# Kernel optimization log

Hardware: AMD Instinct MI355X
Metric: run time of the kernel (lower is better)

The kernel has to match this reference:

```python
import jax, jax.numpy as jnp
import numpy as np

B, T, C = 2, 2048, 2048
N_HEAD, N_GROUPS, HEAD_SIZE = 16, 4, 128
Q_PER_KV = N_HEAD // N_GROUPS  # 4
N_ELEM = HEAD_SIZE  # rotary_percentage = 1.0
HIDDEN = 4 * C
EPS = 1e-5


def layernorm(x, w, b):
    m = jnp.mean(x, axis=-1, keepdims=True)
    v = jnp.mean(jnp.square(x - m), axis=-1, keepdims=True)
    return (x - m) * jax.lax.rsqrt(v + EPS) * w + b


def apply_rope(x, cos, sin):
    # x: [B, H, T, n_elem]; cos/sin: [T, n_elem] (broadcast over B, H)
    d = x.shape[-1]
    x1, x2 = x[..., : d // 2], x[..., d // 2 :]
    rotated = jnp.concatenate((-x2, x1), axis=-1)
    return x * cos + rotated * sin


def setup_inputs() -> dict:
    key = jax.random.key(0)
    ks = jax.random.split(key, 8)
    x = jax.random.normal(ks[0], (B, T, C), dtype=jnp.float32)
    # rope cache (NeoX/LLaMA half-rotation layout), base 10000
    theta = 1.0 / (10000.0 ** (jnp.arange(0, N_ELEM, 2, dtype=jnp.float32) / N_ELEM))
    idx_theta = jnp.outer(jnp.arange(T, dtype=jnp.float32), theta)  # [T, n_elem//2]
    idx_theta = jnp.concatenate((idx_theta, idx_theta), axis=-1)    # [T, n_elem]
    cos, sin = jnp.cos(idx_theta), jnp.sin(idx_theta)
    mask = jnp.tril(jnp.ones((T, T), dtype=bool))[None, None]  # causal [1,1,T,T]
    s = 0.02
    return {
        "x": x,
        "cos": cos,
        "sin": sin,
        "ln1_w": jnp.ones((C,), jnp.float32),
        "ln1_b": jnp.zeros((C,), jnp.float32),
        "ln2_w": jnp.ones((C,), jnp.float32),
        "ln2_b": jnp.zeros((C,), jnp.float32),
        "w_attn": jax.random.normal(ks[1], (C, (N_HEAD + 2 * N_GROUPS) * HEAD_SIZE), jnp.float32) * s,
        "w_proj": jax.random.normal(ks[2], (C, C), jnp.float32) * s,
        "w_fc": jax.random.normal(ks[3], (C, HIDDEN), jnp.float32) * s,
        "w_mlp_proj": jax.random.normal(ks[4], (HIDDEN, C), jnp.float32) * s,
        "mask": mask,
    }


def reference(x, cos, sin, ln1_w, ln1_b, ln2_w, ln2_b, w_attn, w_proj, w_fc, w_mlp_proj, mask):
    n1 = layernorm(x, ln1_w, ln1_b)
    # fused QKV projection
    qkv = n1 @ w_attn  # [B, T, (H + 2G) * hs]
    qkv = qkv.reshape(B, T, N_GROUPS, Q_PER_KV + 2, HEAD_SIZE)
    q = qkv[:, :, :, :Q_PER_KV]      # [B, T, G, qpk, hs]
    k = qkv[:, :, :, Q_PER_KV]       # [B, T, G, hs]
    v = qkv[:, :, :, Q_PER_KV + 1]   # [B, T, G, hs]
    # q -> [B, H, T, hs] (group-major head order)
    q = q.transpose(0, 2, 3, 1, 4).reshape(B, N_HEAD, T, HEAD_SIZE)
    # k, v -> [B, G, T, hs] then repeat_interleave groups to H heads
    k = jnp.repeat(k.transpose(0, 2, 1, 3), Q_PER_KV, axis=1)  # [B, H, T, hs]
    v = jnp.repeat(v.transpose(0, 2, 1, 3), Q_PER_KV, axis=1)
    # RoPE on the first N_ELEM dims (here full head)
    q = jnp.concatenate((apply_rope(q[..., :N_ELEM], cos, sin), q[..., N_ELEM:]), axis=-1)
    k = jnp.concatenate((apply_rope(k[..., :N_ELEM], cos, sin), k[..., N_ELEM:]), axis=-1)
    scale = 1.0 / np.sqrt(HEAD_SIZE).astype(np.float32)
    att = jnp.einsum("bhtd,bhsd->bhts", q, k) * scale
    att = jnp.where(mask, att, jnp.finfo(att.dtype).min)
    att = jax.nn.softmax(att, axis=-1)
    y = jnp.einsum("bhts,bhsd->bhtd", att, v)
    y = y.transpose(0, 2, 1, 3).reshape(B, T, C)
    h = y @ w_proj
    # non-parallel residual (LLaMA-style): x + attn, then x + mlp(norm2(x))
    x = x + h
    n2 = layernorm(x, ln2_w, ln2_b)
    mlp = jax.nn.gelu(n2 @ w_fc, approximate=False) @ w_mlp_proj
    return x + mlp
```

## Files before the change

kernel.cpp:

```cpp
#include <hip/hip_runtime.h>
#include <stdint.h>
#include <math.h>

#define Tn   2048
#define Cn   2048
#define BTn  4096
#define NQKV 3072
#define HID  8192

typedef unsigned short u16;
typedef float f32x4 __attribute__((ext_vector_type(4)));
typedef short s16x8 __attribute__((ext_vector_type(8)));

__device__ __forceinline__ float b2f(u16 u) { return __uint_as_float(((unsigned)u) << 16); }
__device__ __forceinline__ u16 f2b(float f) {
  unsigned i = __float_as_uint(f);
  return (u16)((i + 0x7fffu + ((i >> 16) & 1u)) >> 16);
}

__device__ __forceinline__ void g2l16(const void* g, void* l) {
  __builtin_amdgcn_global_load_lds((const __attribute__((address_space(1))) unsigned int*)g,
                                   (__attribute__((address_space(3))) unsigned int*)l,
                                   16, 0, 0);
}

__global__ __launch_bounds__(256) void transpose_f2b(const float* __restrict__ in,
                                                     u16* __restrict__ out, int R, int C) {
  __shared__ float tile[32][33];
  int bx = blockIdx.x * 32, by = blockIdx.y * 32;
  int tx = threadIdx.x, ty = threadIdx.y;
  #pragma unroll
  for (int j = 0; j < 32; j += 8)
    tile[ty + j][tx] = in[(size_t)(by + ty + j) * C + bx + tx];
  __syncthreads();
  #pragma unroll
  for (int j = 0; j < 32; j += 8)
    out[(size_t)(bx + ty + j) * R + by + tx] = f2b(tile[tx][ty + j]);
}

__global__ __launch_bounds__(256) void transpose_u16(const u16* __restrict__ in,
                                                     u16* __restrict__ out, int R, int C) {
  __shared__ u16 tile[32][33];
  const size_t zb = (size_t)blockIdx.z * R * C;
  int bx = blockIdx.x * 32, by = blockIdx.y * 32;
  int tx = threadIdx.x, ty = threadIdx.y;
  #pragma unroll
  for (int j = 0; j < 32; j += 8)
    tile[ty + j][tx] = in[zb + (size_t)(by + ty + j) * C + bx + tx];
  __syncthreads();
  #pragma unroll
  for (int j = 0; j < 32; j += 8)
    out[zb + (size_t)(bx + ty + j) * R + by + tx] = tile[tx][ty + j];
}

__global__ __launch_bounds__(256)
void layernorm_k(const float* __restrict__ x, const float* __restrict__ w,
                 const float* __restrict__ bb, u16* __restrict__ out) {
  __shared__ float red[256];
  __shared__ float sm, sv;
  const int tid = threadIdx.x;
  const long row = blockIdx.x;
  const float* xr = x + row * (long)Cn;
  float v[8];
  float s = 0.f;
  #pragma unroll
  for (int i = 0; i < 8; ++i) { v[i] = xr[i * 256 + tid]; s += v[i]; }
  red[tid] = s; __syncthreads();
  for (int st = 128; st > 0; st >>= 1) { if (tid < st) red[tid] += red[tid + st]; __syncthreads(); }
  if (tid == 0) sm = red[0] * (1.f / Cn);
  __syncthreads();
  const float mean = sm;
  float s2 = 0.f;
  #pragma unroll
  for (int i = 0; i < 8; ++i) { float d = v[i] - mean; s2 += d * d; }
  red[tid] = s2; __syncthreads();
  for (int st = 128; st > 0; st >>= 1) { if (tid < st) red[tid] += red[tid + st]; __syncthreads(); }
  if (tid == 0) sv = rsqrtf(red[0] * (1.f / Cn) + 1e-5f);
  __syncthreads();
  const float rstd = sv;
  #pragma unroll
  for (int i = 0; i < 8; ++i) {
    int c = i * 256 + tid;
    out[row * (long)Cn + c] = f2b((v[i] - mean) * rstd * w[c] + bb[c]);
  }
}

__global__ __launch_bounds__(256)
void rope_split(const u16* __restrict__ qkv, const float* __restrict__ cs,
                const float* __restrict__ sn, u16* __restrict__ q,
                u16* __restrict__ k, u16* __restrict__ v) {
  const long idx = (long)blockIdx.x * 256 + threadIdx.x;
  const int row = (int)(idx / NQKV);
  const int col = (int)(idx % NQKV);
  const int b = row >> 11, t = row & 2047;
  const int g = col / 768, rr = col % 768, s = rr >> 7, d = rr & 127;
  const u16 raw = qkv[idx];
  if (s == 5) { v[((long)(b * 4 + g) * Tn + t) * 128 + d] = raw; return; }
  const float xv = b2f(raw);
  const float x2 = b2f(qkv[idx - d + (d ^ 64)]);
  const float c = cs[t * 128 + d];
  const float si = sn[t * 128 + d];
  const float rot = (d < 64) ? -x2 : x2;
  const float o = xv * c + rot * si;
  if (s == 4) k[((long)(b * 4 + g) * Tn + t) * 128 + d] = f2b(o);
  else        q[((long)(b * 16 + g * 4 + s) * Tn + t) * 128 + d] = f2b(o);
}

__global__ __launch_bounds__(256, 2)
void attn_flash(const u16* __restrict__ q, const u16* __restrict__ k,
                const u16* __restrict__ vt, u16* __restrict__ y) {
  __shared__ __align__(16) u16 Ks[4 * 64 * 32];
  __shared__ __align__(16) u16 Vs[2 * 128 * 32];
  __shared__ __align__(16) u16 Ps[4][2 * 16 * 32];
  const int tid = threadIdx.x, wave = tid >> 6, lane = tid & 63;
  const int fr = lane & 15, quad = lane >> 4;
  const int lr4 = lane >> 2, lc8 = (lane & 3) << 3;
  const int bx = blockIdx.x, bh = blockIdx.y;
  const int b = bh >> 4, h = bh & 15, g = h >> 2;
  const int bg = b * 4 + g;
  const u16* kg = k + (size_t)bg * Tn * 128;
  const u16* vg = vt + (size_t)bg * 128 * Tn;
  const int q0 = bx * 64 + wave * 16;

  s16x8 qf[4];
  {
    const u16* qrow = q + ((size_t)bh * Tn + q0 + fr) * 128;
    #pragma unroll
    for (int kc = 0; kc < 4; ++kc)
      qf[kc] = *(const s16x8*)(qrow + kc * 32 + quad * 8);
  }
  f32x4 o_acc[8] = {};
  float m_r[4], l_r[4];
  #pragma unroll
  for (int r = 0; r < 4; ++r) { m_r[r] = -1e30f; l_r[r] = 0.f; }
  const float scale = 0.08838834764831845f;

  for (int step = 0; step <= bx; ++step) {
    const int j0 = step * 64;
    __syncthreads();
    #pragma unroll
    for (int kc = 0; kc < 4; ++kc)
      g2l16(kg + (size_t)(j0 + wave * 16 + lr4) * 128 + kc * 32 + lc8,
            Ks + kc * 2048 + wave * 16 * 32);
    #pragma unroll
    for (int kc = 0; kc < 2; ++kc)
      #pragma unroll
      for (int hh = 0; hh < 2; ++hh)
        g2l16(vg + (size_t)(wave * 32 + hh * 16 + lr4) * Tn + j0 + kc * 32 + lc8,
              Vs + kc * 4096 + (wave * 32 + hh * 16) * 32);
    __syncthreads();

    f32x4 s[4] = {};
    #pragma unroll
    for (int kc = 0; kc < 4; ++kc)
      #pragma unroll
      for (int nt = 0; nt < 4; ++nt) {
        s16x8 bf = *(const s16x8*)(Ks + kc * 2048 + (nt * 16 + fr) * 32 + quad * 8);
        s[nt] = __builtin_amdgcn_mfma_f32_16x16x32_bf16(qf[kc], bf, s[nt], 0, 0, 0);
      }

    const bool diag = (step == bx);
    #pragma unroll
    for (int r = 0; r < 4; ++r) {
      float vmax = -1e30f;
      #pragma unroll
      for (int nt = 0; nt < 4; ++nt) {
        float sv = s[nt][r] * scale;
        if (diag && (j0 + nt * 16 + fr) > (q0 + quad * 4 + r)) sv = -1e30f;
        s[nt][r] = sv;
        vmax = fmaxf(vmax, sv);
      }
      #pragma unroll
      for (int mk = 1; mk < 16; mk <<= 1) vmax = fmaxf(vmax, __shfl_xor(vmax, mk, 64));
      const float mnew = fmaxf(m_r[r], vmax);
      const float alpha = __expf(m_r[r] - mnew);
      float rsum = 0.f;
      #pragma unroll
      for (int nt = 0; nt < 4; ++nt) {
        float pv = __expf(s[nt][r] - mnew);
        s[nt][r] = pv; rsum += pv;
      }
      #pragma unroll
      for (int mk = 1; mk < 16; mk <<= 1) rsum += __shfl_xor(rsum, mk, 64);
      l_r[r] = l_r[r] * alpha + rsum;
      m_r[r] = mnew;
      #pragma unroll
      for (int nt = 0; nt < 8; ++nt) o_acc[nt][r] *= alpha;
    }

    u16* pw = Ps[wave];
    #pragma unroll
    for (int nt = 0; nt < 4; ++nt) {
      const int col = nt * 16 + fr, pan = col >> 5, cc = col & 31;
      #pragma unroll
      for (int r = 0; r < 4; ++r)
        pw[pan * 512 + (quad * 4 + r) * 32 + cc] = f2b(s[nt][r]);
    }
    #pragma unroll
    for (int kc = 0; kc < 2; ++kc) {
      s16x8 af = *(const s16x8*)(pw + kc * 512 + fr * 32 + quad * 8);
      #pragma unroll
      for (int nt = 0; nt < 8; ++nt) {
        s16x8 bf = *(const s16x8*)(Vs + kc * 4096 + (nt * 16 + fr) * 32 + quad * 8);
        o_acc[nt] = __builtin_amdgcn_mfma_f32_16x16x32_bf16(af, bf, o_acc[nt], 0, 0, 0);
      }
    }
  }

  #pragma unroll
  for (int r = 0; r < 4; ++r) {
    const float inv = 1.f / l_r[r];
    const size_t row = (size_t)(b * Tn + q0 + quad * 4 + r) * Cn + h * 128;
    #pragma unroll
    for (int nt = 0; nt < 8; ++nt)
      y[row + nt * 16 + fr] = f2b(o_acc[nt][r] * inv);
  }
}

template <int EPI>
__global__ __launch_bounds__(256, 2)
void gemm_bt(const u16* __restrict__ A, const u16* __restrict__ Bt,
             const float* __restrict__ res, u16* __restrict__ ob,
             float* __restrict__ of, int M, int N, int K, int num_n) {
  __shared__ __align__(16) u16 As[128 * 32];
  __shared__ __align__(16) u16 Bs[128 * 32];
  const int pid = blockIdx.x;
  const int xcd = pid & 7, idx = pid >> 3;
  const int j = idx & 15;
  const int gp = (idx >> 4) * 8 + xcd;
  const int npc = num_n >> 2;
  const int pr = gp / npc, pc = gp - pr * npc;
  const long m0 = (long)(pr * 4 + (j & 3)) * 128;
  const long n0 = (long)(pc * 4 + (j >> 2)) * 128;

  const int tid = threadIdx.x;
  const int wave = tid >> 6, lane = tid & 63;
  const int wy = wave >> 1, wx = wave & 1;
  const int lr = lane >> 2;
  const int lc = (lane & 3) << 3;
  const int fr = lane & 15, quad = lane >> 4;
  f32x4 acc[4][4] = {};

  for (int k0 = 0; k0 < K; k0 += 32) {
    __syncthreads();
    #pragma unroll
    for (int i = 0; i < 2; ++i) {
      const int seg = wave * 2 + i;
      const int row = seg * 16 + lr;
      g2l16(A + (m0 + row) * (long)K + k0 + lc, As + seg * 512);
      g2l16(Bt + (n0 + row) * (long)K + k0 + lc, Bs + seg * 512);
    }
    __syncthreads();
    s16x8 af[4], bfr[4];
    #pragma unroll
    for (int mi = 0; mi < 4; ++mi)
      af[mi] = *(const s16x8*)(As + (wy * 64 + mi * 16 + fr) * 32 + quad * 8);
    #pragma unroll
    for (int ni = 0; ni < 4; ++ni)
      bfr[ni] = *(const s16x8*)(Bs + (wx * 64 + ni * 16 + fr) * 32 + quad * 8);
    #pragma unroll
    for (int mi = 0; mi < 4; ++mi)
      #pragma unroll
      for (int ni = 0; ni < 4; ++ni)
        acc[mi][ni] = __builtin_amdgcn_mfma_f32_16x16x32_bf16(af[mi], bfr[ni], acc[mi][ni], 0, 0, 0);
  }

  #pragma unroll
  for (int mi = 0; mi < 4; ++mi)
    #pragma unroll
    for (int ni = 0; ni < 4; ++ni)
      #pragma unroll
      for (int r = 0; r < 4; ++r) {
        const long row = m0 + wy * 64 + mi * 16 + quad * 4 + r;
        const long col = n0 + wx * 64 + ni * 16 + fr;
        const long idx2 = row * N + col;
        const float vv = acc[mi][ni][r];
        if (EPI == 0) ob[idx2] = f2b(vv);
        else if (EPI == 1) of[idx2] = vv + res[idx2];
        else ob[idx2] = f2b(0.5f * vv * (1.0f + erff(vv * 0.70710678118654752f)));
      }
}

extern "C" void kernel_launch(void* const* d_in, const int* in_sizes, int n_in,
                              void* d_out, int out_size, void* d_ws, size_t ws_size,
                              hipStream_t stream) {
  (void)in_sizes; (void)n_in; (void)out_size; (void)ws_size;
  const float* x      = (const float*)d_in[0];
  const float* cosb   = (const float*)d_in[1];
  const float* sinb   = (const float*)d_in[2];
  const float* ln1w   = (const float*)d_in[3];
  const float* ln1b   = (const float*)d_in[4];
  const float* ln2w   = (const float*)d_in[5];
  const float* ln2b   = (const float*)d_in[6];
  const float* w_attn = (const float*)d_in[7];
  const float* w_proj = (const float*)d_in[8];
  const float* w_fc   = (const float*)d_in[9];
  const float* w_mp   = (const float*)d_in[10];
  float* out = (float*)d_out;

  char* p = (char*)d_ws;
  auto alloc = [&](size_t bytes) { char* r = p; p += (bytes + 255) & ~(size_t)255; return (void*)r; };
  u16*  wT_attn = (u16*)alloc((size_t)NQKV * Cn * 2);
  u16*  wT_proj = (u16*)alloc((size_t)Cn * Cn * 2);
  u16*  wT_fc   = (u16*)alloc((size_t)HID * Cn * 2);
  u16*  wT_mp   = (u16*)alloc((size_t)Cn * HID * 2);
  u16*  n12     = (u16*)alloc((size_t)BTn * Cn * 2);
  u16*  qkv     = (u16*)alloc((size_t)BTn * NQKV * 2);
  u16*  qb      = (u16*)alloc((size_t)2 * 16 * Tn * 128 * 2);
  u16*  kb      = (u16*)alloc((size_t)2 * 4 * Tn * 128 * 2);
  u16*  vb      = (u16*)alloc((size_t)2 * 4 * Tn * 128 * 2);
  float* x1     = (float*)alloc((size_t)BTn * Cn * 4);
  u16*  hbuf    = (u16*)alloc((size_t)BTn * HID * 2);
  u16*  vt      = n12;

  dim3 tb(32, 8);
  transpose_f2b<<<dim3(NQKV / 32, Cn / 32), tb, 0, stream>>>(w_attn, wT_attn, Cn, NQKV);
  transpose_f2b<<<dim3(Cn / 32, Cn / 32), tb, 0, stream>>>(w_proj, wT_proj, Cn, Cn);
  transpose_f2b<<<dim3(HID / 32, Cn / 32), tb, 0, stream>>>(w_fc, wT_fc, Cn, HID);
  transpose_f2b<<<dim3(Cn / 32, HID / 32), tb, 0, stream>>>(w_mp, wT_mp, HID, Cn);

  layernorm_k<<<BTn, 256, 0, stream>>>(x, ln1w, ln1b, n12);
  gemm_bt<0><<<(BTn / 128) * (NQKV / 128), 256, 0, stream>>>(n12, wT_attn, nullptr, qkv, nullptr, BTn, NQKV, Cn, NQKV / 128);
  rope_split<<<(int)(((long)BTn * NQKV) / 256), 256, 0, stream>>>(qkv, cosb, sinb, qb, kb, vb);
  transpose_u16<<<dim3(128 / 32, Tn / 32, 8), tb, 0, stream>>>(vb, vt, Tn, 128);
  attn_flash<<<dim3(Tn / 64, 32), 256, 0, stream>>>(qb, kb, vt, qkv );
  gemm_bt<1><<<(BTn / 128) * (Cn / 128), 256, 0, stream>>>(qkv, wT_proj, x, nullptr, x1, BTn, Cn, Cn, Cn / 128);
  layernorm_k<<<BTn, 256, 0, stream>>>(x1, ln2w, ln2b, n12);
  gemm_bt<2><<<(BTn / 128) * (HID / 128), 256, 0, stream>>>(n12, wT_fc, nullptr, hbuf, nullptr, BTn, HID, Cn, HID / 128);
  gemm_bt<1><<<(BTn / 128) * (Cn / 128), 256, 0, stream>>>(hbuf, wT_mp, x1, nullptr, out, BTn, Cn, HID, Cn / 128);
}
```

Measured before the change: 919.6 us.

## Replace 128x128 GEMM with double-buffered 256x256 tile, swizzled LDS, 8 waves

Replaces the simple single-buffered 128x128x32 bf16 GEMM with a 256x256 tile, 512-thread kernel using 128 KB of LDS. It double-buffers K=64 stages and interleaves async global->LDS loads with MFMA phases under explicit waitcnt, barriers and setprio. It also XOR-swizzles the LDS layout to avoid bank conflicts. The aim is to hide load latency and raise operand reuse for the four big GEMMs, at the cost of fewer blocks and very tight manual synchronisation. The smaller grids (e.g. 128 blocks for the projection GEMMs) risk underfilling the GPU's compute units.

```diff
diff --git a/kernel.cpp b/kernel.cpp
--- a/kernel.cpp
+++ b/kernel.cpp
@@ -217,62 +217,125 @@
   }
 }
 
+#define BAR  __builtin_amdgcn_s_barrier()
+#define LG0  asm volatile("s_waitcnt lgkmcnt(0)" ::: "memory")
+#define RD_A(BUF, MI4)                                                                  \
+  { _Pragma("unroll") for (int m_ = 0; m_ < 4; ++m_) {                                  \
+      _Pragma("unroll") for (int k_ = 0; k_ < 2; ++k_)                                  \
+        ar[m_][k_] = *(const s16x8*)(Sb + (BUF) * 32768 + aBase +                       \
+                                     (((MI4) + m_) << 11) + (k_ << 10) + fragoff); } }
+#define RD_B(BUF, NI2, DST)                                                             \
+  { _Pragma("unroll") for (int n_ = 0; n_ < 2; ++n_) {                                  \
+      _Pragma("unroll") for (int k_ = 0; k_ < 2; ++k_)                                  \
+        DST[n_][k_] = *(const s16x8*)(Sb + (BUF) * 32768 + bBase +                      \
+                                      (((NI2) + n_) << 11) + (k_ << 10) + fragoff); } }
+#define MM(MB, NB, BR)                                                                  \
+  { __builtin_amdgcn_s_setprio(1);                                                     \
+    _Pragma("unroll") for (int m_ = 0; m_ < 4; ++m_) {                                  \
+      _Pragma("unroll") for (int n_ = 0; n_ < 2; ++n_) {                                \
+        _Pragma("unroll") for (int k_ = 0; k_ < 2; ++k_)                                \
+          acc[(MB) + m_][(NB) + n_] = __builtin_amdgcn_mfma_f32_16x16x32_bf16(          \
+              ar[m_][k_], BR[n_][k_], acc[(MB) + m_][(NB) + n_], 0, 0, 0); } }          \
+    __builtin_amdgcn_s_setprio(0); }
+
 template <int EPI>
-__global__ __launch_bounds__(256, 2)
-void gemm_bt(const u16* __restrict__ A, const u16* __restrict__ Bt,
+__global__ __launch_bounds__(512, 2)
+void gemm256(const u16* __restrict__ A, const u16* __restrict__ Bt,
              const float* __restrict__ res, u16* __restrict__ ob,
              float* __restrict__ of, int M, int N, int K, int num_n) {
-  __shared__ __align__(16) u16 As[128 * 32];
-  __shared__ __align__(16) u16 Bs[128 * 32];
+  __shared__ __align__(16) u16 S[65536];
+  char* Sb = (char*)S;
+  (void)M;
+
   const int pid = blockIdx.x;
   const int xcd = pid & 7, idx = pid >> 3;
-  const int j = idx & 15;
-  const int gp = (idx >> 4) * 8 + xcd;
-  const int npc = num_n >> 2;
+  const int jj = idx & 3;
+  const int gp = (idx >> 2) * 8 + xcd;
+  const int npc = num_n >> 1;
   const int pr = gp / npc, pc = gp - pr * npc;
-  const long m0 = (long)(pr * 4 + (j & 3)) * 128;
-  const long n0 = (long)(pc * 4 + (j >> 2)) * 128;
-
-  const int tid = threadIdx.x;
+  const long m0 = (long)(pr * 2 + (jj >> 1)) * 256;
+  const long n0 = (long)(pc * 2 + (jj & 1)) * 256;
+
+  const int tid = (int)threadIdx.x;
   const int wave = tid >> 6, lane = tid & 63;
-  const int wy = wave >> 1, wx = wave & 1;
-  const int lr = lane >> 2;
-  const int lc = (lane & 3) << 3;
+  const int wr = wave >> 2, wc = wave & 3;
   const int fr = lane & 15, quad = lane >> 4;
-  f32x4 acc[4][4] = {};
-
-  for (int k0 = 0; k0 < K; k0 += 32) {
-    __syncthreads();
-    #pragma unroll
-    for (int i = 0; i < 2; ++i) {
-      const int seg = wave * 2 + i;
-      const int row = seg * 16 + lr;
-      g2l16(A + (m0 + row) * (long)K + k0 + lc, As + seg * 512);
-      g2l16(Bt + (n0 + row) * (long)K + k0 + lc, Bs + seg * 512);
-    }
-    __syncthreads();
-    s16x8 af[4], bfr[4];
-    #pragma unroll
-    for (int mi = 0; mi < 4; ++mi)
-      af[mi] = *(const s16x8*)(As + (wy * 64 + mi * 16 + fr) * 32 + quad * 8);
+  const int fragoff = (fr * 64 + quad * 16) ^ (((fr >> 3) & 1) << 5);
+  const int aBase = wr * 16384;
+  const int bBase = 65536 + (wc >> 1) * 16384 + ((wc & 1) << 13);
+
+  int srow[2], skcb[2];
+  #pragma unroll
+  for (int rr = 0; rr < 2; ++rr) {
+    const int d = rr * 8192 + wave * 1024 + lane * 16;
+    const int l = d ^ (((d >> 9) & 1) << 5);
+    srow[rr] = ((l >> 11) << 4) | ((l >> 6) & 15);
+    skcb[rr] = (((l >> 10) & 1) << 6) | (l & 63);
+  }
+  auto stage = [&](const u16* __restrict__ src, long grow0, int kt, int regionByte) {
+    #pragma unroll
+    for (int rr = 0; rr < 2; ++rr)
+      g2l16((const char*)src + (grow0 + srow[rr]) * (long)K * 2 + (long)kt * 128 + skcb[rr],
+            Sb + regionByte + rr * 8192 + wave * 1024);
+  };
+
+  const int nk = K >> 6;
+  const int nk2 = nk >> 1;
+
+  stage(A,  m0,       0, 0);
+  stage(A,  m0 + 128, 0, 16384);
+  stage(Bt, n0,       0, 65536);
+  stage(Bt, n0 + 128, 0, 81920);
+  stage(Bt, n0,       1, 98304);
+  stage(Bt, n0 + 128, 1, 114688);
+  asm volatile("s_waitcnt vmcnt(4)" ::: "memory");
+  BAR;
+
+  s16x8 ar[4][2], br0[2][2], br1[2][2];
+  f32x4 acc[8][4] = {};
+
+  for (int i = 0; i < nk2; ++i) {
+    const int t1 = 2 * i + 1, s0 = 2 * i + 2, s1 = 2 * i + 3;
+    const bool v0 = (s0 < nk), v1 = (s1 < nk);
+    RD_A(0, 0); RD_B(0, 0, br0);
+    stage(A, m0, t1, 32768);
+    asm volatile("s_waitcnt lgkmcnt(8)" ::: "memory");
+    BAR; LG0; MM(0, 0, br0); BAR;
+    RD_B(0, 2, br1);
+    stage(A, m0 + 128, t1, 49152);
+    BAR; LG0; MM(0, 2, br1); BAR;
+    RD_A(0, 4);
+    if (v0) stage(Bt, n0, s0, 65536);
+    BAR; LG0; MM(4, 2, br1); BAR;
+    if (v0) stage(Bt, n0 + 128, s0, 81920);
+    BAR; LG0; MM(4, 0, br0);
+    if (v0) { asm volatile("s_waitcnt vmcnt(4)" ::: "memory"); }
+    else    { asm volatile("s_waitcnt vmcnt(0)" ::: "memory"); }
+    BAR;
+    RD_A(1, 0); RD_B(1, 0, br0);
+    if (v0) stage(A, m0, s0, 0);
+    asm volatile("s_waitcnt lgkmcnt(8)" ::: "memory");
+    BAR; LG0; MM(0, 0, br0); BAR;
+    RD_B(1, 2, br1);
+    if (v0) stage(A, m0 + 128, s0, 16384);
+    BAR; LG0; MM(0, 2, br1); BAR;
+    RD_A(1, 4);
+    if (v1) stage(Bt, n0, s1, 98304);
+    BAR; LG0; MM(4, 2, br1); BAR;
+    if (v1) stage(Bt, n0 + 128, s1, 114688);
+    BAR; LG0; MM(4, 0, br0);
+    asm volatile("s_waitcnt vmcnt(4)" ::: "memory");
+    BAR;
+  }
+
+  #pragma unroll
+  for (int mi = 0; mi < 8; ++mi)
     #pragma unroll
     for (int ni = 0; ni < 4; ++ni)
-      bfr[ni] = *(const s16x8*)(Bs + (wx * 64 + ni * 16 + fr) * 32 + quad * 8);
-    #pragma unroll
-    for (int mi = 0; mi < 4; ++mi)
-      #pragma unroll
-      for (int ni = 0; ni < 4; ++ni)
-        acc[mi][ni] = __builtin_amdgcn_mfma_f32_16x16x32_bf16(af[mi], bfr[ni], acc[mi][ni], 0, 0, 0);
-  }
-
-  #pragma unroll
-  for (int mi = 0; mi < 4; ++mi)
-    #pragma unroll
-    for (int ni = 0; ni < 4; ++ni)
       #pragma unroll
       for (int r = 0; r < 4; ++r) {
-        const long row = m0 + wy * 64 + mi * 16 + quad * 4 + r;
-        const long col = n0 + wx * 64 + ni * 16 + fr;
+        const long row = m0 + wr * 128 + mi * 16 + quad * 4 + r;
+        const long col = n0 + wc * 64 + ni * 16 + fr;
         const long idx2 = row * N + col;
         const float vv = acc[mi][ni][r];
         if (EPI == 0) ob[idx2] = f2b(vv);
@@ -320,12 +383,12 @@
   transpose_f2b<<<dim3(Cn / 32, HID / 32), tb, 0, stream>>>(w_mp, wT_mp, HID, Cn);
 
   layernorm_k<<<BTn, 256, 0, stream>>>(x, ln1w, ln1b, n12);
-  gemm_bt<0><<<(BTn / 128) * (NQKV / 128), 256, 0, stream>>>(n12, wT_attn, nullptr, qkv, nullptr, BTn, NQKV, Cn, NQKV / 128);
+  gemm256<0><<<(BTn / 256) * (NQKV / 256), 512, 0, stream>>>(n12, wT_attn, nullptr, qkv, nullptr, BTn, NQKV, Cn, NQKV / 256);
   rope_split<<<(int)(((long)BTn * NQKV) / 256), 256, 0, stream>>>(qkv, cosb, sinb, qb, kb, vb);
   transpose_u16<<<dim3(128 / 32, Tn / 32, 8), tb, 0, stream>>>(vb, vt, Tn, 128);
   attn_flash<<<dim3(Tn / 64, 32), 256, 0, stream>>>(qb, kb, vt, qkv );
-  gemm_bt<1><<<(BTn / 128) * (Cn / 128), 256, 0, stream>>>(qkv, wT_proj, x, nullptr, x1, BTn, Cn, Cn, Cn / 128);
+  gemm256<1><<<(BTn / 256) * (Cn / 256), 512, 0, stream>>>(qkv, wT_proj, x, nullptr, x1, BTn, Cn, Cn, Cn / 256);
   layernorm_k<<<BTn, 256, 0, stream>>>(x1, ln2w, ln2b, n12);
-  gemm_bt<2><<<(BTn / 128) * (HID / 128), 256, 0, stream>>>(n12, wT_fc, nullptr, hbuf, nullptr, BTn, HID, Cn, HID / 128);
-  gemm_bt<1><<<(BTn / 128) * (Cn / 128), 256, 0, stream>>>(hbuf, wT_mp, x1, nullptr, out, BTn, Cn, HID, Cn / 128);
-}
+  gemm256<2><<<(BTn / 256) * (HID / 256), 512, 0, stream>>>(n12, wT_fc, nullptr, hbuf, nullptr, BTn, HID, Cn, HID / 256);
+  gemm256<1><<<(BTn / 256) * (Cn / 256), 512, 0, stream>>>(hbuf, wT_mp, x1, nullptr, out, BTn, Cn, HID, Cn / 256);
+}
```

After: 908.4 us. No clear change (-1.2%).
